# Kernel tuning notes

Measured on AMD Instinct MI355X. Metric: run time of the kernel, lower is better.

## Reference

```python
import jax, jax.numpy as jnp
import numpy as np

EMB = 1024
HEADS = 8
INNER = EMB // HEADS          # 128
HEAD_DIM = INNER // HEADS     # 16
SCALE = INNER ** -0.5         # note: module scales by inner_dim, not head_dim
EPS = 1e-5


def setup_inputs() -> dict:
    key = jax.random.key(0)
    ks = jax.random.split(key, 4)
    b, n = 16, 1024
    x = jax.random.normal(ks[0], (b, n, EMB), dtype=jnp.float32)
    gamma = jnp.ones((EMB,), dtype=jnp.float32)
    beta = jnp.zeros((EMB,), dtype=jnp.float32)
    w_qkv = jax.random.normal(ks[1], (EMB, 3 * INNER), dtype=jnp.float32) * (EMB ** -0.5)
    w_proj = jax.random.normal(ks[2], (INNER, EMB), dtype=jnp.float32) * (INNER ** -0.5)
    b_proj = jnp.zeros((EMB,), dtype=jnp.float32)
    return {"x": x, "gamma": gamma, "beta": beta, "w_qkv": w_qkv,
            "w_proj": w_proj, "b_proj": b_proj}


def reference(x, gamma, beta, w_qkv, w_proj, b_proj):
    b, n, _ = x.shape
    # LayerNorm
    mu = jnp.mean(x, axis=-1, keepdims=True)
    var = jnp.var(x, axis=-1, keepdims=True)
    xn = (x - mu) * jax.lax.rsqrt(var + EPS) * gamma + beta
    # QKV projection (bias=False): [b, n, 3*INNER]
    qkv = jnp.einsum('bne,ef->bnf', xn, w_qkv)
    q, k, v = jnp.split(qkv, 3, axis=-1)
    to_heads = lambda a: a.reshape(b, n, HEADS, HEAD_DIM).transpose(0, 2, 1, 3)
    q, k, v = to_heads(q) * SCALE, to_heads(k), to_heads(v)
    # full score matrix [b, h, n, n] (as the original einsum does)
    attn = jax.nn.softmax(jnp.einsum('bhid,bhjd->bhij', q, k), axis=-1)
    out = jnp.einsum('bhij,bhjd->bhid', attn, v)
    out = out.transpose(0, 2, 1, 3).reshape(b, n, INNER)
    return jnp.einsum('bni,ie->bne', out, w_proj) + b_proj
```

## Files before the change

kernel.cpp:

```cpp
#include <hip/hip_runtime.h>

#define LOG2E 1.44269504088896340736f
#define QSCALE (0.08838834764831845f * LOG2E)

using short8 = __attribute__((ext_vector_type(8))) short;
using f32x4  = __attribute__((ext_vector_type(4))) float;
using f32x16 = __attribute__((ext_vector_type(16))) float;

union U16B { uint4 u; short8 s; };

typedef __attribute__((address_space(3))) unsigned char lds_byte;
typedef const __attribute__((address_space(1))) unsigned char glb_byte;
#define GLOAD16(gp, lp) __builtin_amdgcn_global_load_lds((glb_byte*)(gp), (lds_byte*)(lp), 16, 0, 0)

static __device__ __forceinline__ unsigned short f2bf(float f){
  union { float f; unsigned int i; } c; c.f = f;
  unsigned int i = c.i;
  i += 0x7fffu + ((i >> 16) & 1u);
  return (unsigned short)(i >> 16);
}

__global__ __launch_bounds__(256) void k_cvtw(const float* __restrict__ wqkv,
                                              const float* __restrict__ wproj,
                                              unsigned short* __restrict__ wqkvT,
                                              unsigned short* __restrict__ wprojT){
  int t = blockIdx.x*256 + threadIdx.x;
  if (t < 49152){
    int n = t>>7, k0 = (t&127)*8;
    float sc = (n < 128) ? QSCALE : 1.0f;
    const float* src = wqkv + (size_t)k0*384 + n;
    ushort4 lo, hi;
    lo.x = f2bf(src[0]*sc);    lo.y = f2bf(src[384]*sc);
    lo.z = f2bf(src[768]*sc);  lo.w = f2bf(src[1152]*sc);
    hi.x = f2bf(src[1536]*sc); hi.y = f2bf(src[1920]*sc);
    hi.z = f2bf(src[2304]*sc); hi.w = f2bf(src[2688]*sc);
    *(ushort4*)(wqkvT + (size_t)n*1024 + k0)     = lo;
    *(ushort4*)(wqkvT + (size_t)n*1024 + k0 + 4) = hi;
  } else {
    int t2 = t - 49152;
    int n = t2>>4, k0 = (t2&15)*8;
    const float* src = wproj + (size_t)k0*1024 + n;
    ushort4 lo, hi;
    lo.x = f2bf(src[0]);    lo.y = f2bf(src[1024]);
    lo.z = f2bf(src[2048]); lo.w = f2bf(src[3072]);
    hi.x = f2bf(src[4096]); hi.y = f2bf(src[5120]);
    hi.z = f2bf(src[6144]); hi.w = f2bf(src[7168]);
    *(ushort4*)(wprojT + (size_t)n*128 + k0)     = lo;
    *(ushort4*)(wprojT + (size_t)n*128 + k0 + 4) = hi;
  }
}

__global__ __launch_bounds__(256) void k_ln(const float* __restrict__ x,
                                            const float* __restrict__ gamma,
                                            const float* __restrict__ beta,
                                            unsigned short* __restrict__ xn){
  const int tok = (blockIdx.x*256 + threadIdx.x) >> 6;
  const int l = threadIdx.x & 63;
  const float4* xr = (const float4*)(x + (size_t)tok*1024);
  float4 v[4];
  #pragma unroll
  for (int i=0;i<4;i++) v[i] = xr[l + i*64];
  float s = 0.f, s2 = 0.f;
  #pragma unroll
  for (int i=0;i<4;i++){
    s  += v[i].x+v[i].y+v[i].z+v[i].w;
    s2 += v[i].x*v[i].x+v[i].y*v[i].y+v[i].z*v[i].z+v[i].w*v[i].w;
  }
  #pragma unroll
  for (int o=32;o;o>>=1){ s += __shfl_xor(s,o); s2 += __shfl_xor(s2,o); }
  float mu   = s*(1.0f/1024.0f);
  float rstd = rsqrtf(s2*(1.0f/1024.0f) - mu*mu + 1e-5f);
  ushort4* xo = (ushort4*)(xn + (size_t)tok*1024);
  #pragma unroll
  for (int i=0;i<4;i++){
    float4 g = ((const float4*)gamma)[l + i*64];
    float4 b = ((const float4*)beta)[l + i*64];
    ushort4 o;
    o.x = f2bf((v[i].x-mu)*rstd*g.x + b.x);
    o.y = f2bf((v[i].y-mu)*rstd*g.y + b.y);
    o.z = f2bf((v[i].z-mu)*rstd*g.z + b.z);
    o.w = f2bf((v[i].w-mu)*rstd*g.w + b.w);
    xo[l + i*64] = o;
  }
}

__global__ __launch_bounds__(256) void k_qkv(const unsigned short* __restrict__ xn,
                                             const unsigned short* __restrict__ wT,
                                             unsigned short* __restrict__ q,
                                             unsigned short* __restrict__ kbuf,
                                             unsigned short* __restrict__ vT){
  __shared__ __align__(16) unsigned short sm[64*64 + 128*64];
  unsigned short* sA = sm;
  unsigned short* sB = sm + 4096;
  const int tid = threadIdx.x;
  const int w = tid>>6, l = tid&63;
  const int m0 = blockIdx.x*64;
  const int sec = blockIdx.y;
  const int nb = sec*128;
  const int wm = (w>>1)*32, wn = (w&1)*64;
  f32x4 acc[2][4] = {};
  for (int k0=0; k0<1024; k0+=64){
    #pragma unroll
    for (int i=0;i<2;i++){
      int chunk = i*256 + tid;
      int row = chunk>>3;
      int ch = (tid&7) ^ (row&7);
      GLOAD16(xn + (size_t)(m0+row)*1024 + k0 + ch*8,
              (char*)sA + (i*256 + w*64)*16);
    }
    #pragma unroll
    for (int i=0;i<4;i++){
      int chunk = i*256 + tid;
      int row = chunk>>3;
      int ch = (tid&7) ^ (row&7);
      GLOAD16(wT + (size_t)(nb+row)*1024 + k0 + ch*8,
              (char*)sB + (i*256 + w*64)*16);
    }
    __syncthreads();
    #pragma unroll
    for (int s=0; s<2; ++s){
      short8 af[2], bfr[4];
      #pragma unroll
      for (int i=0;i<2;i++){
        int row = wm + i*16 + (l&15);
        U16B ta; ta.u = *(const uint4*)((const char*)sA + row*128 + ((s*64 + (l>>4)*16) ^ ((row&7)<<4)));
        af[i] = ta.s;
      }
      #pragma unroll
      for (int j=0;j<4;j++){
        int col = wn + j*16 + (l&15);
        U16B tb; tb.u = *(const uint4*)((const char*)sB + col*128 + ((s*64 + (l>>4)*16) ^ ((col&7)<<4)));
        bfr[j] = tb.s;
      }
      #pragma unroll
      for (int i=0;i<2;i++)
        #pragma unroll
        for (int j=0;j<4;j++)
          acc[i][j] = __builtin_amdgcn_mfma_f32_16x16x32_bf16(af[i], bfr[j], acc[i][j], 0,0,0);
    }
    __syncthreads();
  }
  const int b  = m0 >> 10;
  const int n0 = m0 & 1023;
  if (sec < 2){
    #pragma unroll
    for (int fm=0; fm<2; ++fm)
      #pragma unroll
      for (int fn=0; fn<4; ++fn){
        int colf = wn + fn*16 + (l&15);
        #pragma unroll
        for (int i=0;i<4;i++){
          int row = wm + fm*16 + (l>>4)*4 + i;
          *(unsigned short*)((char*)sm + row*256 + ((2*colf) ^ ((row&15)<<4))) = f2bf(acc[fm][fn][i]);
        }
      }
    __syncthreads();
    unsigned short* dst = (sec==0) ? q : kbuf;
    #pragma unroll
    for (int it=0; it<4; ++it){
      int chunk = it*256 + tid;
      int tokl = chunk>>4, cc = chunk&15;
      uint4 vv = *(const uint4*)((const char*)sm + tokl*256 + ((cc*16) ^ ((tokl&15)<<4)));
      int h = cc>>1, d0 = (cc&1)*8;
      *(uint4*)(dst + ((size_t)(b*8 + h)*1024 + n0 + tokl)*16 + d0) = vv;
    }
  } else {
    #pragma unroll
    for (int fm=0; fm<2; ++fm)
      #pragma unroll
      for (int fn=0; fn<4; ++fn){
        int colf = wn + fn*16 + (l&15);
        int r0 = wm + fm*16 + (l>>4)*4;
        ushort4 pk;
        pk.x = f2bf(acc[fm][fn][0]); pk.y = f2bf(acc[fm][fn][1]);
        pk.z = f2bf(acc[fm][fn][2]); pk.w = f2bf(acc[fm][fn][3]);
        *(ushort4*)((char*)sm + colf*128 + ((2*r0) ^ ((colf&7)<<4))) = pk;
      }
    __syncthreads();
    #pragma unroll
    for (int it=0; it<4; ++it){
      int chunk = it*256 + tid;
      int f = chunk>>3, cc = chunk&7;
      uint4 vv = *(const uint4*)((const char*)sm + f*128 + ((cc*16) ^ ((f&7)<<4)));
      int h = f>>4, d = f&15;
      unsigned short* dp = vT + ((size_t)(b*8 + h)*16 + d)*1024 + n0 + (cc>>1)*16 + (cc&1)*4;
      *(uint2*)dp       = make_uint2(vv.x, vv.y);
      *(uint2*)(dp + 8) = make_uint2(vv.z, vv.w);
    }
  }
}

__global__ __launch_bounds__(256) void k_attn(const unsigned short* __restrict__ q,
                                              const unsigned short* __restrict__ kbuf,
                                              const unsigned short* __restrict__ vT,
                                              unsigned short* __restrict__ aout){
  const int bh = blockIdx.x;
  const int qc = blockIdx.y;
  const int w = threadIdx.x>>6, l = threadIdx.x&63;
  const int l31 = l&31, hi = l>>5;
  const int h = bh & 7;
  const int qrow = qc*128 + w*32 + l31;
  U16B qf_u; qf_u.u = *(const uint4*)(q + ((size_t)bh*1024 + qrow)*16 + hi*8);
  const short8 qf = qf_u.s;
  const unsigned short* kptr = kbuf + (size_t)bh*1024*16 + (size_t)l31*16 + hi*8;
  const unsigned short* vptr = vT + (size_t)bh*16*1024 + (size_t)(l31 & 15)*1024 + hi*8;
  const bool vok = (l31 < 16);
  const unsigned int ob = ((l31==16)||(l31==20)) ? 0x3F803F80u : 0u;
  const uint4 cvu = make_uint4(ob, ob, ob, ob);
  f32x16 acc = {};
  U16B kf; kf.u = *(const uint4*)kptr; kptr += 512;
  U16B v0, v1; v0.u = cvu; v1.u = cvu;
  if (vok){ v0.u = *(const uint4*)vptr; v1.u = *(const uint4*)(vptr + 16); }
  vptr += 32;
  #pragma unroll 2
  for (int t=0; t<32; ++t){
    U16B kn; kn.u = *(const uint4*)kptr; kptr += 512;
    U16B v0n, v1n; v0n.u = cvu; v1n.u = cvu;
    if (vok){ v0n.u = *(const uint4*)vptr; v1n.u = *(const uint4*)(vptr + 16); }
    vptr += 32;
    f32x16 zz = {};
    f32x16 sv = __builtin_amdgcn_mfma_f32_32x32x16_bf16(kf.s, qf, zz, 0,0,0);
    float p[16];
    #pragma unroll
    for (int r=0;r<16;r++){ p[r] = __builtin_amdgcn_exp2f(sv[r]); }
    unsigned int u[8];
    #pragma unroll
    for (int j=0;j<8;j++){
      asm("v_cvt_pk_bf16_f32 %0, %1, %2" : "=v"(u[j]) : "v"(p[2*j]), "v"(p[2*j+1]));
    }
    U16B p0, p1;
    p0.u.x = u[0]; p0.u.y = u[1]; p0.u.z = u[2]; p0.u.w = u[3];
    p1.u.x = u[4]; p1.u.y = u[5]; p1.u.z = u[6]; p1.u.w = u[7];
    acc = __builtin_amdgcn_mfma_f32_32x32x16_bf16(v0.s, p0.s, acc, 0,0,0);
    acc = __builtin_amdgcn_mfma_f32_32x32x16_bf16(v1.s, p1.s, acc, 0,0,0);
    kf = kn; v0 = v0n; v1 = v1n;
  }
  float inv = 1.0f/acc[8];
  const size_t tok = (size_t)(bh>>3)*1024 + qrow;
  ushort4 o;
  o.x = f2bf(acc[0]*inv); o.y = f2bf(acc[1]*inv); o.z = f2bf(acc[2]*inv); o.w = f2bf(acc[3]*inv);
  *(ushort4*)(aout + tok*128 + h*16 + hi*4) = o;
  o.x = f2bf(acc[4]*inv); o.y = f2bf(acc[5]*inv); o.z = f2bf(acc[6]*inv); o.w = f2bf(acc[7]*inv);
  *(ushort4*)(aout + tok*128 + h*16 + 8 + hi*4) = o;
}

__global__ __launch_bounds__(256) void k_proj(const unsigned short* __restrict__ aout,
                                              const unsigned short* __restrict__ wT,
                                              const float* __restrict__ bias,
                                              float* __restrict__ out){
  __shared__ __align__(16) unsigned short sA[128*128];
  __shared__ __align__(16) unsigned short sB[128*128];
  const int tid = threadIdx.x;
  const int w = tid>>6, l = tid&63;
  const int m0 = blockIdx.x*128, nb = blockIdx.y*128;
  #pragma unroll
  for (int i=0;i<8;i++){
    int chunk = i*256 + tid;
    int row = chunk>>4;
    int ch = (tid&15) ^ (row&15);
    GLOAD16(aout + (size_t)(m0+row)*128 + ch*8, (char*)sA + (i*256 + w*64)*16);
  }
  #pragma unroll
  for (int i=0;i<8;i++){
    int chunk = i*256 + tid;
    int row = chunk>>4;
    int ch = (tid&15) ^ (row&15);
    GLOAD16(wT + (size_t)(nb+row)*128 + ch*8, (char*)sB + (i*256 + w*64)*16);
  }
  __syncthreads();
  const int wm = (w>>1)*64, wn = (w&1)*64;
  f32x4 acc[4][4] = {};
  #pragma unroll
  for (int s=0; s<4; ++s){
    short8 af[4], bfr[4];
    #pragma unroll
    for (int i=0;i<4;i++){
      int row = wm + i*16 + (l&15);
      U16B ta; ta.u = *(const uint4*)((const char*)sA + row*256 + ((s*64 + (l>>4)*16) ^ ((row&15)<<4)));
      af[i] = ta.s;
      int col = wn + i*16 + (l&15);
      U16B tb; tb.u = *(const uint4*)((const char*)sB + col*256 + ((s*64 + (l>>4)*16) ^ ((col&15)<<4)));
      bfr[i] = tb.s;
    }
    #pragma unroll
    for (int i=0;i<4;i++)
      #pragma unroll
      for (int j=0;j<4;j++)
        acc[i][j] = __builtin_amdgcn_mfma_f32_16x16x32_bf16(af[i], bfr[j], acc[i][j], 0,0,0);
  }
  #pragma unroll
  for (int fn=0; fn<4; ++fn){
    int col = nb + wn + fn*16 + (l&15);
    float bv = bias[col];
    #pragma unroll
    for (int fm=0; fm<4; ++fm)
      #pragma unroll
      for (int i=0;i<4;i++)
        out[(size_t)(m0 + wm + fm*16 + (l>>4)*4 + i)*1024 + col] = acc[fm][fn][i] + bv;
  }
}

extern "C" void kernel_launch(void* const* d_in, const int* in_sizes, int n_in,
                              void* d_out, int out_size, void* d_ws, size_t ws_size,
                              hipStream_t stream){
  (void)in_sizes; (void)n_in; (void)out_size; (void)ws_size;
  const float* x     = (const float*)d_in[0];
  const float* gamma = (const float*)d_in[1];
  const float* beta  = (const float*)d_in[2];
  const float* wqkv  = (const float*)d_in[3];
  const float* wproj = (const float*)d_in[4];
  const float* bias  = (const float*)d_in[5];
  float* out = (float*)d_out;
  char* ws = (char*)d_ws;
  unsigned short* xn = (unsigned short*)ws;
  unsigned short* q  = (unsigned short*)(ws + 33554432);
  unsigned short* kb = (unsigned short*)(ws + 33554432 + 4194304);
  unsigned short* vT = (unsigned short*)(ws + 33554432 + 2*4194304);
  unsigned short* ao = (unsigned short*)(ws + 33554432 + 3*4194304);
  unsigned short* wqkvT = (unsigned short*)(ws + 33554432 + 4*4194304);
  unsigned short* wprojT = (unsigned short*)(ws + 33554432 + 4*4194304 + 786432);
  k_cvtw<<<dim3(256), dim3(256), 0, stream>>>(wqkv, wproj, wqkvT, wprojT);
  k_ln  <<<dim3(4096), dim3(256), 0, stream>>>(x, gamma, beta, xn);
  k_qkv <<<dim3(256,3), dim3(256), 0, stream>>>(xn, wqkvT, q, kb, vT);
  k_attn<<<dim3(128,8), dim3(256), 0, stream>>>(q, kb, vT, ao);
  k_proj<<<dim3(128,8), dim3(256), 0, stream>>>(ao, wprojT, bias, out);
}
```

Baseline: 91.82 us.

## Merge weight conversion into LN, double-buffer QKV GEMM, software-pipeline attention

Result: faster. 89.88 us (-2.1%).

```diff
diff --git a/kernel.cpp b/kernel.cpp
--- a/kernel.cpp
+++ b/kernel.cpp
@@ -20,67 +20,68 @@
   return (unsigned short)(i >> 16);
 }
 
-__global__ __launch_bounds__(256) void k_cvtw(const float* __restrict__ wqkv,
-                                              const float* __restrict__ wproj,
-                                              unsigned short* __restrict__ wqkvT,
-                                              unsigned short* __restrict__ wprojT){
-  int t = blockIdx.x*256 + threadIdx.x;
-  if (t < 49152){
-    int n = t>>7, k0 = (t&127)*8;
-    float sc = (n < 128) ? QSCALE : 1.0f;
-    const float* src = wqkv + (size_t)k0*384 + n;
-    ushort4 lo, hi;
-    lo.x = f2bf(src[0]*sc);    lo.y = f2bf(src[384]*sc);
-    lo.z = f2bf(src[768]*sc);  lo.w = f2bf(src[1152]*sc);
-    hi.x = f2bf(src[1536]*sc); hi.y = f2bf(src[1920]*sc);
-    hi.z = f2bf(src[2304]*sc); hi.w = f2bf(src[2688]*sc);
-    *(ushort4*)(wqkvT + (size_t)n*1024 + k0)     = lo;
-    *(ushort4*)(wqkvT + (size_t)n*1024 + k0 + 4) = hi;
-  } else {
-    int t2 = t - 49152;
-    int n = t2>>4, k0 = (t2&15)*8;
-    const float* src = wproj + (size_t)k0*1024 + n;
-    ushort4 lo, hi;
-    lo.x = f2bf(src[0]);    lo.y = f2bf(src[1024]);
-    lo.z = f2bf(src[2048]); lo.w = f2bf(src[3072]);
-    hi.x = f2bf(src[4096]); hi.y = f2bf(src[5120]);
-    hi.z = f2bf(src[6144]); hi.w = f2bf(src[7168]);
-    *(ushort4*)(wprojT + (size_t)n*128 + k0)     = lo;
-    *(ushort4*)(wprojT + (size_t)n*128 + k0 + 4) = hi;
-  }
-}
-
 __global__ __launch_bounds__(256) void k_ln(const float* __restrict__ x,
                                             const float* __restrict__ gamma,
                                             const float* __restrict__ beta,
-                                            unsigned short* __restrict__ xn){
-  const int tok = (blockIdx.x*256 + threadIdx.x) >> 6;
-  const int l = threadIdx.x & 63;
-  const float4* xr = (const float4*)(x + (size_t)tok*1024);
-  float4 v[4];
-  #pragma unroll
-  for (int i=0;i<4;i++) v[i] = xr[l + i*64];
-  float s = 0.f, s2 = 0.f;
-  #pragma unroll
-  for (int i=0;i<4;i++){
-    s  += v[i].x+v[i].y+v[i].z+v[i].w;
-    s2 += v[i].x*v[i].x+v[i].y*v[i].y+v[i].z*v[i].z+v[i].w*v[i].w;
-  }
-  #pragma unroll
-  for (int o=32;o;o>>=1){ s += __shfl_xor(s,o); s2 += __shfl_xor(s2,o); }
-  float mu   = s*(1.0f/1024.0f);
-  float rstd = rsqrtf(s2*(1.0f/1024.0f) - mu*mu + 1e-5f);
-  ushort4* xo = (ushort4*)(xn + (size_t)tok*1024);
-  #pragma unroll
-  for (int i=0;i<4;i++){
-    float4 g = ((const float4*)gamma)[l + i*64];
-    float4 b = ((const float4*)beta)[l + i*64];
-    ushort4 o;
-    o.x = f2bf((v[i].x-mu)*rstd*g.x + b.x);
-    o.y = f2bf((v[i].y-mu)*rstd*g.y + b.y);
-    o.z = f2bf((v[i].z-mu)*rstd*g.z + b.z);
-    o.w = f2bf((v[i].w-mu)*rstd*g.w + b.w);
-    xo[l + i*64] = o;
+                                            unsigned short* __restrict__ xn,
+                                            const float* __restrict__ wqkv,
+                                            const float* __restrict__ wproj,
+                                            unsigned short* __restrict__ wqkvT,
+                                            unsigned short* __restrict__ wprojT){
+  if (blockIdx.x < 4096){
+    const int tok = (blockIdx.x*256 + threadIdx.x) >> 6;
+    const int l = threadIdx.x & 63;
+    const float4* xr = (const float4*)(x + (size_t)tok*1024);
+    float4 v[4];
+    #pragma unroll
+    for (int i=0;i<4;i++) v[i] = xr[l + i*64];
+    float s = 0.f, s2 = 0.f;
+    #pragma unroll
+    for (int i=0;i<4;i++){
+      s  += v[i].x+v[i].y+v[i].z+v[i].w;
+      s2 += v[i].x*v[i].x+v[i].y*v[i].y+v[i].z*v[i].z+v[i].w*v[i].w;
+    }
+    #pragma unroll
+    for (int o=32;o;o>>=1){ s += __shfl_xor(s,o); s2 += __shfl_xor(s2,o); }
+    float mu   = s*(1.0f/1024.0f);
+    float rstd = rsqrtf(s2*(1.0f/1024.0f) - mu*mu + 1e-5f);
+    ushort4* xo = (ushort4*)(xn + (size_t)tok*1024);
+    #pragma unroll
+    for (int i=0;i<4;i++){
+      float4 g = ((const float4*)gamma)[l + i*64];
+      float4 b = ((const float4*)beta)[l + i*64];
+      ushort4 o;
+      o.x = f2bf((v[i].x-mu)*rstd*g.x + b.x);
+      o.y = f2bf((v[i].y-mu)*rstd*g.y + b.y);
+      o.z = f2bf((v[i].z-mu)*rstd*g.z + b.z);
+      o.w = f2bf((v[i].w-mu)*rstd*g.w + b.w);
+      xo[l + i*64] = o;
+    }
+  } else {
+    int t = (blockIdx.x - 4096)*256 + threadIdx.x;
+    if (t < 49152){
+      int n = t>>7, k0 = (t&127)*8;
+      float sc = (n < 128) ? QSCALE : 1.0f;
+      const float* src = wqkv + (size_t)k0*384 + n;
+      ushort4 lo, hi;
+      lo.x = f2bf(src[0]*sc);    lo.y = f2bf(src[384]*sc);
+      lo.z = f2bf(src[768]*sc);  lo.w = f2bf(src[1152]*sc);
+      hi.x = f2bf(src[1536]*sc); hi.y = f2bf(src[1920]*sc);
+      hi.z = f2bf(src[2304]*sc); hi.w = f2bf(src[2688]*sc);
+      *(ushort4*)(wqkvT + (size_t)n*1024 + k0)     = lo;
+      *(ushort4*)(wqkvT + (size_t)n*1024 + k0 + 4) = hi;
+    } else {
+      int t2 = t - 49152;
+      int n = t2>>4, k0 = (t2&15)*8;
+      const float* src = wproj + (size_t)k0*1024 + n;
+      ushort4 lo, hi;
+      lo.x = f2bf(src[0]);    lo.y = f2bf(src[1024]);
+      lo.z = f2bf(src[2048]); lo.w = f2bf(src[3072]);
+      hi.x = f2bf(src[4096]); hi.y = f2bf(src[5120]);
+      hi.z = f2bf(src[6144]); hi.w = f2bf(src[7168]);
+      *(ushort4*)(wprojT + (size_t)n*128 + k0)     = lo;
+      *(ushort4*)(wprojT + (size_t)n*128 + k0 + 4) = hi;
+    }
   }
 }
 
@@ -89,9 +90,7 @@
                                              unsigned short* __restrict__ q,
                                              unsigned short* __restrict__ kbuf,
                                              unsigned short* __restrict__ vT){
-  __shared__ __align__(16) unsigned short sm[64*64 + 128*64];
-  unsigned short* sA = sm;
-  unsigned short* sB = sm + 4096;
+  __shared__ __align__(16) unsigned short sm[2][64*64 + 128*64];
   const int tid = threadIdx.x;
   const int w = tid>>6, l = tid&63;
   const int m0 = blockIdx.x*64;
@@ -99,7 +98,10 @@
   const int nb = sec*128;
   const int wm = (w>>1)*32, wn = (w&1)*64;
   f32x4 acc[2][4] = {};
-  for (int k0=0; k0<1024; k0+=64){
+
+  auto stage = [&](int buf, int k0){
+    unsigned short* sA = &sm[buf][0];
+    unsigned short* sB = &sm[buf][4096];
     #pragma unroll
     for (int i=0;i<2;i++){
       int chunk = i*256 + tid;
@@ -116,7 +118,20 @@
       GLOAD16(wT + (size_t)(nb+row)*1024 + k0 + ch*8,
               (char*)sB + (i*256 + w*64)*16);
     }
-    __syncthreads();
+  };
+
+  stage(0, 0);
+  for (int t=0; t<16; ++t){
+    const int cur = t & 1;
+    if (t < 15){
+      stage(cur^1, (t+1)<<6);
+      asm volatile("s_waitcnt vmcnt(6)" ::: "memory");
+    } else {
+      asm volatile("s_waitcnt vmcnt(0)" ::: "memory");
+    }
+    __builtin_amdgcn_s_barrier();
+    const unsigned short* sA = &sm[cur][0];
+    const unsigned short* sB = &sm[cur][4096];
     #pragma unroll
     for (int s=0; s<2; ++s){
       short8 af[2], bfr[4];
@@ -138,10 +153,12 @@
         for (int j=0;j<4;j++)
           acc[i][j] = __builtin_amdgcn_mfma_f32_16x16x32_bf16(af[i], bfr[j], acc[i][j], 0,0,0);
     }
-    __syncthreads();
-  }
+    __builtin_amdgcn_s_barrier();
+  }
+
   const int b  = m0 >> 10;
   const int n0 = m0 & 1023;
+  unsigned short* ep = &sm[0][0];
   if (sec < 2){
     #pragma unroll
     for (int fm=0; fm<2; ++fm)
@@ -151,7 +168,7 @@
         #pragma unroll
         for (int i=0;i<4;i++){
           int row = wm + fm*16 + (l>>4)*4 + i;
-          *(unsigned short*)((char*)sm + row*256 + ((2*colf) ^ ((row&15)<<4))) = f2bf(acc[fm][fn][i]);
+          *(unsigned short*)((char*)ep + row*256 + ((2*colf) ^ ((row&15)<<4))) = f2bf(acc[fm][fn][i]);
         }
       }
     __syncthreads();
@@ -160,7 +177,7 @@
     for (int it=0; it<4; ++it){
       int chunk = it*256 + tid;
       int tokl = chunk>>4, cc = chunk&15;
-      uint4 vv = *(const uint4*)((const char*)sm + tokl*256 + ((cc*16) ^ ((tokl&15)<<4)));
+      uint4 vv = *(const uint4*)((const char*)ep + tokl*256 + ((cc*16) ^ ((tokl&15)<<4)));
       int h = cc>>1, d0 = (cc&1)*8;
       *(uint4*)(dst + ((size_t)(b*8 + h)*1024 + n0 + tokl)*16 + d0) = vv;
     }
@@ -174,14 +191,14 @@
         ushort4 pk;
         pk.x = f2bf(acc[fm][fn][0]); pk.y = f2bf(acc[fm][fn][1]);
         pk.z = f2bf(acc[fm][fn][2]); pk.w = f2bf(acc[fm][fn][3]);
-        *(ushort4*)((char*)sm + colf*128 + ((2*r0) ^ ((colf&7)<<4))) = pk;
+        *(ushort4*)((char*)ep + colf*128 + ((2*r0) ^ ((colf&7)<<4))) = pk;
       }
     __syncthreads();
     #pragma unroll
     for (int it=0; it<4; ++it){
       int chunk = it*256 + tid;
       int f = chunk>>3, cc = chunk&7;
-      uint4 vv = *(const uint4*)((const char*)sm + f*128 + ((cc*16) ^ ((f&7)<<4)));
+      uint4 vv = *(const uint4*)((const char*)ep + f*128 + ((cc*16) ^ ((f&7)<<4)));
       int h = f>>4, d = f&15;
       unsigned short* dp = vT + ((size_t)(b*8 + h)*16 + d)*1024 + n0 + (cc>>1)*16 + (cc&1)*4;
       *(uint2*)dp       = make_uint2(vv.x, vv.y);
@@ -208,32 +225,36 @@
   const unsigned int ob = ((l31==16)||(l31==20)) ? 0x3F803F80u : 0u;
   const uint4 cvu = make_uint4(ob, ob, ob, ob);
   f32x16 acc = {};
+  const f32x16 zz = {};
+
   U16B kf; kf.u = *(const uint4*)kptr; kptr += 512;
+  U16B kn; kn.u = *(const uint4*)kptr; kptr += 512;
   U16B v0, v1; v0.u = cvu; v1.u = cvu;
   if (vok){ v0.u = *(const uint4*)vptr; v1.u = *(const uint4*)(vptr + 16); }
   vptr += 32;
-  #pragma unroll 2
+  f32x16 sv = __builtin_amdgcn_mfma_f32_32x32x16_bf16(kf.s, qf, zz, 0,0,0);
+
   for (int t=0; t<32; ++t){
-    U16B kn; kn.u = *(const uint4*)kptr; kptr += 512;
+    U16B knn; knn.u = *(const uint4*)kptr; kptr += 512;
     U16B v0n, v1n; v0n.u = cvu; v1n.u = cvu;
     if (vok){ v0n.u = *(const uint4*)vptr; v1n.u = *(const uint4*)(vptr + 16); }
     vptr += 32;
-    f32x16 zz = {};
-    f32x16 sv = __builtin_amdgcn_mfma_f32_32x32x16_bf16(kf.s, qf, zz, 0,0,0);
-    float p[16];
-    #pragma unroll
-    for (int r=0;r<16;r++){ p[r] = __builtin_amdgcn_exp2f(sv[r]); }
+    f32x16 svn = __builtin_amdgcn_mfma_f32_32x32x16_bf16(kn.s, qf, zz, 0,0,0);
     unsigned int u[8];
     #pragma unroll
     for (int j=0;j<8;j++){
-      asm("v_cvt_pk_bf16_f32 %0, %1, %2" : "=v"(u[j]) : "v"(p[2*j]), "v"(p[2*j+1]));
+      float a = __builtin_amdgcn_exp2f(sv[2*j]);
+      float b = __builtin_amdgcn_exp2f(sv[2*j+1]);
+      asm("v_cvt_pk_bf16_f32 %0, %1, %2" : "=v"(u[j]) : "v"(a), "v"(b));
     }
     U16B p0, p1;
     p0.u.x = u[0]; p0.u.y = u[1]; p0.u.z = u[2]; p0.u.w = u[3];
     p1.u.x = u[4]; p1.u.y = u[5]; p1.u.z = u[6]; p1.u.w = u[7];
+    __builtin_amdgcn_s_setprio(1);
     acc = __builtin_amdgcn_mfma_f32_32x32x16_bf16(v0.s, p0.s, acc, 0,0,0);
     acc = __builtin_amdgcn_mfma_f32_32x32x16_bf16(v1.s, p1.s, acc, 0,0,0);
-    kf = kn; v0 = v0n; v1 = v1n;
+    __builtin_amdgcn_s_setprio(0);
+    sv = svn; kn = knn; v0 = v0n; v1 = v1n;
   }
   float inv = 1.0f/acc[8];
   const size_t tok = (size_t)(bh>>3)*1024 + qrow;
@@ -319,8 +340,7 @@
   unsigned short* ao = (unsigned short*)(ws + 33554432 + 3*4194304);
   unsigned short* wqkvT = (unsigned short*)(ws + 33554432 + 4*4194304);
   unsigned short* wprojT = (unsigned short*)(ws + 33554432 + 4*4194304 + 786432);
-  k_cvtw<<<dim3(256), dim3(256), 0, stream>>>(wqkv, wproj, wqkvT, wprojT);
-  k_ln  <<<dim3(4096), dim3(256), 0, stream>>>(x, gamma, beta, xn);
+  k_ln  <<<dim3(4352), dim3(256), 0, stream>>>(x, gamma, beta, xn, wqkv, wproj, wqkvT, wprojT);
   k_qkv <<<dim3(256,3), dim3(256), 0, stream>>>(xn, wqkvT, q, kb, vT);
   k_attn<<<dim3(128,8), dim3(256), 0, stream>>>(q, kb, vT, ao);
   k_proj<<<dim3(128,8), dim3(256), 0, stream>>>(ao, wprojT, bias, out);
```
